# Performance work log

Measured on AMD Instinct MI355X. Metric: run time of the kernel, lower is better.

## Reference

```python
import jax, jax.numpy as jnp
import numpy as np

B, T, C, H = 4, 2048, 768, 12
D = C // H  # head_size = 64
ROPE_BASE = 10000.0


def rotary_tables(seq_len, dim, dtype=jnp.float32):
    # dim = head_size; uses dim//2 frequencies
    inv_freq = 1.0 / (ROPE_BASE ** (jnp.arange(0, dim, 2, dtype=jnp.float32) / dim))
    t = jnp.arange(seq_len, dtype=jnp.float32)
    freqs = jnp.outer(t, inv_freq)  # [T, D/2]
    return jnp.cos(freqs).astype(dtype), jnp.sin(freqs).astype(dtype)


def apply_rotary(x, cos, sin):
    # x: [B, H, T, D]; cos/sin: [T, D/2] broadcast over B,H
    d = x.shape[-1] // 2
    x1, x2 = x[..., :d], x[..., d:]
    y1 = x1 * cos + x2 * sin
    y2 = -x1 * sin + x2 * cos
    return jnp.concatenate([y1, y2], axis=-1)


def setup_inputs() -> dict:
    key = jax.random.key(0)
    ks = jax.random.split(key, 5)
    x = jax.random.normal(ks[0], (B, T, C), dtype=jnp.float32)
    W_attn = jax.random.normal(ks[1], (C, 3 * C), dtype=jnp.float32) * (1.0 / np.sqrt(C))
    b_attn = jax.random.normal(ks[2], (3 * C,), dtype=jnp.float32) * 0.02
    W_proj = jax.random.normal(ks[3], (C, C), dtype=jnp.float32) * (1.0 / np.sqrt(C))
    b_proj = jax.random.normal(ks[4], (C,), dtype=jnp.float32) * 0.02
    return {"x": x, "W_attn": W_attn, "b_attn": b_attn, "W_proj": W_proj, "b_proj": b_proj}


def reference(x, W_attn, b_attn, W_proj, b_proj):
    Bx, Tx, Cx = x.shape
    qkv = x @ W_attn + b_attn  # [B, T, 3C]
    q, k, v = jnp.split(qkv, 3, axis=-1)
    # [B, T, C] -> [B, H, T, D]
    to_heads = lambda a: a.reshape(Bx, Tx, H, D).transpose(0, 2, 1, 3)
    q, k, v = to_heads(q), to_heads(k), to_heads(v)
    cos, sin = rotary_tables(Tx, D, x.dtype)
    q = apply_rotary(q, cos, sin)
    k = apply_rotary(k, cos, sin)
    scale = 1.0 / np.sqrt(D)
    scores = jnp.einsum('bhqd,bhkd->bhqk', q, k) * scale  # [B, H, T, T]
    causal = jnp.tril(jnp.ones((Tx, Tx), dtype=bool))
    scores = jnp.where(causal, scores, jnp.finfo(scores.dtype).min)
    attn = jax.nn.softmax(scores, axis=-1)
    y = jnp.einsum('bhqk,bhkd->bhqd', attn, v)  # [B, H, T, D]
    y = y.transpose(0, 2, 1, 3).reshape(Bx, Tx, Cx)
    return y @ W_proj + b_proj
```

## Files before the change

kernel.cpp:

```cpp
#include <hip/hip_runtime.h>
#include <hip/hip_bf16.h>

#define BB 4
#define TT 2048
#define CC 768
#define HH 12
#define DD 64
#define MM (BB * TT)
#define BH (BB * HH)

typedef __bf16 bf16_t;
typedef __bf16 bf16x8 __attribute__((ext_vector_type(8)));
typedef __bf16 bf16x4 __attribute__((ext_vector_type(4)));
typedef float f32x4 __attribute__((ext_vector_type(4)));
typedef float f32x16 __attribute__((ext_vector_type(16)));

__device__ __forceinline__ float fast_exp2(float x) {
#if __has_builtin(__builtin_amdgcn_exp2f)
    return __builtin_amdgcn_exp2f(x);
#else
    return exp2f(x);
#endif
}

__device__ __forceinline__ uint32_t pk2(float lo, float hi) {
    bf16_t l = (bf16_t)lo, h = (bf16_t)hi;
    uint16_t lu = __builtin_bit_cast(uint16_t, l);
    uint16_t hu = __builtin_bit_cast(uint16_t, h);
    return ((uint32_t)hu << 16) | lu;
}

__device__ __forceinline__ void gload_lds16(const void* g, void* l) {
    __builtin_amdgcn_global_load_lds(
        (const __attribute__((address_space(1))) uint32_t*)g,
        (__attribute__((address_space(3))) uint32_t*)l, 16, 0, 0);
}

__global__ void cvt_f32_bf16(const float* __restrict__ in, bf16_t* __restrict__ out, int n4) {
    int tid = blockIdx.x * blockDim.x + threadIdx.x;
    if (tid >= n4) return;
    float4 v = ((const float4*)in)[tid];
    bf16x4 o;
    o[0] = (bf16_t)v.x; o[1] = (bf16_t)v.y; o[2] = (bf16_t)v.z; o[3] = (bf16_t)v.w;
    ((bf16x4*)out)[tid] = o;
}

__global__ void transpose_cvt(const float* __restrict__ W, bf16_t* __restrict__ WT, int K, int N) {
    __shared__ bf16_t tile[32][33];
    int k0 = blockIdx.x * 32, n0 = blockIdx.y * 32;
    int tx = threadIdx.x, ty = threadIdx.y;
#pragma unroll
    for (int r = 0; r < 4; ++r) {
        int kl = ty * 4 + r;
        tile[kl][tx] = (bf16_t)W[(size_t)(k0 + kl) * N + n0 + tx];
    }
    __syncthreads();
#pragma unroll
    for (int r = 0; r < 4; ++r) {
        int nl = ty * 4 + r;
        WT[(size_t)(n0 + nl) * K + k0 + tx] = tile[tx][nl];
    }
}

#define GEMM_CORE(A_, BT_, acc_)                                                       \
    __shared__ bf16_t As[2][128 * 32];                                                 \
    __shared__ bf16_t Bs[2][128 * 32];                                                 \
    int tid = threadIdx.x;                                                             \
    int wv = tid >> 6, lane = tid & 63, c = lane & 15, quad = lane >> 4;               \
    int wm = (wv >> 1) * 64, wn = (wv & 1) * 64;                                       \
    int m0 = blockIdx.x * 128, n0 = blockIdx.y * 128;                                  \
    int srow = wv * 32 + (lane >> 2);                                                  \
    int slot = lane & 3;                                                               \
    auto stage = [&](int buf, int k0) {                                                \
        _Pragma("unroll")                                                              \
        for (int ins = 0; ins < 2; ++ins) {                                            \
            int r = srow + ins * 16;                                                   \
            int g = (slot - ((r >> 1) & 3)) & 3;                                       \
            const bf16_t* ga = A_ + (size_t)(m0 + r) * K + k0 + g * 8;                 \
            const bf16_t* gb = BT_ + (size_t)(n0 + r) * K + k0 + g * 8;                \
            gload_lds16(ga, &As[buf][(wv * 32 + ins * 16) * 32]);                      \
            gload_lds16(gb, &Bs[buf][(wv * 32 + ins * 16) * 32]);                      \
        }                                                                              \
    };                                                                                 \
    int s_rd = (quad + ((c >> 1) & 3)) & 3;                                            \
    const int nk = K / 32;                                                             \
    stage(0, 0);                                                                       \
    for (int kt = 0; kt < nk; ++kt) {                                                  \
        __syncthreads();                                                               \
        if (kt + 1 < nk) stage((kt + 1) & 1, (kt + 1) * 32);                           \
        int buf = kt & 1;                                                              \
        bf16x8 af[4], bfr[4];                                                          \
        _Pragma("unroll")                                                              \
        for (int i = 0; i < 4; ++i) af[i] = *(const bf16x8*)&As[buf][(wm + i * 16 + c) * 32 + s_rd * 8];  \
        _Pragma("unroll")                                                              \
        for (int j = 0; j < 4; ++j) bfr[j] = *(const bf16x8*)&Bs[buf][(wn + j * 16 + c) * 32 + s_rd * 8]; \
        _Pragma("unroll")                                                              \
        for (int i = 0; i < 4; ++i)                                                    \
            _Pragma("unroll")                                                          \
            for (int j = 0; j < 4; ++j)                                                \
                acc_[i][j] = __builtin_amdgcn_mfma_f32_16x16x32_bf16(af[i], bfr[j], acc_[i][j], 0, 0, 0); \
    }

__global__ __launch_bounds__(256, 3) void gemm_qkv(
        const bf16_t* __restrict__ A, const bf16_t* __restrict__ BT,
        const float* __restrict__ bias,
        bf16_t* __restrict__ Qh, bf16_t* __restrict__ Kh, bf16_t* __restrict__ Vt) {
    const int K = 768;
    __shared__ __align__(16) bf16_t smem[17408];
    bf16_t* Asp = smem;
    bf16_t* Bsp = smem + 8192;
    int tid = threadIdx.x;
    int wv = tid >> 6, lane = tid & 63, c = lane & 15, quad = lane >> 4;
    int wm = (wv >> 1) * 64, wn = (wv & 1) * 64;
    int m0 = blockIdx.x * 128, n0 = blockIdx.y * 128;
    int srow = wv * 32 + (lane >> 2);
    int slot = lane & 3;
    auto stage = [&](int buf, int k0) {
#pragma unroll
        for (int ins = 0; ins < 2; ++ins) {
            int r = srow + ins * 16;
            int g = (slot - ((r >> 1) & 3)) & 3;
            gload_lds16(A + (size_t)(m0 + r) * K + k0 + g * 8, &Asp[buf * 4096 + (wv * 32 + ins * 16) * 32]);
            gload_lds16(BT + (size_t)(n0 + r) * K + k0 + g * 8, &Bsp[buf * 4096 + (wv * 32 + ins * 16) * 32]);
        }
    };
    int s_rd = (quad + ((c >> 1) & 3)) & 3;
    f32x4 acc[4][4] = {};
    const int nk = K / 32;
    stage(0, 0);
    for (int kt = 0; kt < nk; ++kt) {
        __syncthreads();
        if (kt + 1 < nk) stage((kt + 1) & 1, (kt + 1) * 32);
        int buf = kt & 1;
        bf16x8 af[4], bfr[4];
#pragma unroll
        for (int i = 0; i < 4; ++i) af[i] = *(const bf16x8*)&Asp[buf * 4096 + (wm + i * 16 + c) * 32 + s_rd * 8];
#pragma unroll
        for (int j = 0; j < 4; ++j) bfr[j] = *(const bf16x8*)&Bsp[buf * 4096 + (wn + j * 16 + c) * 32 + s_rd * 8];
#pragma unroll
        for (int i = 0; i < 4; ++i)
#pragma unroll
            for (int j = 0; j < 4; ++j)
                acc[i][j] = __builtin_amdgcn_mfma_f32_16x16x32_bf16(af[i], bfr[j], acc[i][j], 0, 0, 0);
    }
    __syncthreads();

    int type = n0 / 768;
    int hloc = ((n0 % 768) + wn) >> 6;
    int bidx = m0 >> 11;
    int colb = n0 + wn;
    int tb = (m0 + wm) & (TT - 1);
    bf16_t* epi = smem + wv * 4352;
    int rrow = lane >> 3, cchunk = lane & 7;

    if (type < 2) {
        const float rscale = (type == 0) ? 0.125f * 1.44269504088896f : 1.0f;
#pragma unroll
        for (int j = 0; j < 2; ++j) {
            int dlo = j * 16 + c;
            float infr = fast_exp2(-(float)dlo * 0.4152410118609828f);
            float blo = bias[colb + j * 16 + c];
            float bhi = bias[colb + (j + 2) * 16 + c];
#pragma unroll
            for (int i = 0; i < 4; ++i)
#pragma unroll
                for (int r = 0; r < 4; ++r) {
                    int lr = i * 16 + quad * 4 + r;
                    float a = acc[i][j][r] + blo;
                    float b2 = acc[i][j + 2][r] + bhi;
                    float fr = (float)(tb + lr) * infr;
                    float cs, sn;
                    __sincosf(fr, &sn, &cs);
                    epi[lr * 68 + dlo]      = (bf16_t)((a * cs + b2 * sn) * rscale);
                    epi[lr * 68 + dlo + 32] = (bf16_t)((-a * sn + b2 * cs) * rscale);
                }
        }
        bf16_t* dst = (type == 0 ? Qh : Kh) + (size_t)(bidx * HH + hloc) * TT * DD + (size_t)tb * DD;
#pragma unroll
        for (int it = 0; it < 8; ++it) {
            int row = it * 8 + rrow;
            bf16x8 v = *(const bf16x8*)&epi[row * 68 + cchunk * 8];
            *(bf16x8*)&dst[row * 64 + cchunk * 8] = v;
        }
    } else {
        int kt64 = tb >> 6;
#pragma unroll
        for (int j = 0; j < 4; ++j) {
            int dim = j * 16 + c;
            float bv = bias[colb + j * 16 + c];
            int rot = (dim & 7) * 8;
#pragma unroll
            for (int i = 0; i < 4; ++i)
#pragma unroll
                for (int r = 0; r < 4; ++r) {
                    int tin = i * 16 + quad * 4 + r;
                    epi[dim * 68 + ((tin + rot) & 63)] = (bf16_t)(acc[i][j][r] + bv);
                }
        }
        bf16_t* dstV = Vt + (size_t)(bidx * HH + hloc) * (TT / 64) * 4096 + (size_t)kt64 * 4096;
#pragma unroll
        for (int it = 0; it < 8; ++it) {
            int dim = it * 8 + rrow;
            int src = ((cchunk + (dim & 7)) & 7) * 8;
            bf16x8 v = *(const bf16x8*)&epi[dim * 68 + src];
            *(bf16x8*)&dstV[dim * 64 + cchunk * 8] = v;
        }
    }
}

__global__ __launch_bounds__(256, 3) void gemm_proj(
        const bf16_t* __restrict__ A, const bf16_t* __restrict__ BT,
        const float* __restrict__ bias, float* __restrict__ Cout) {
    const int K = 768;
    f32x4 acc[4][4] = {};
    GEMM_CORE(A, BT, acc)
#pragma unroll
    for (int j = 0; j < 4; ++j) {
        int col = n0 + wn + j * 16 + c;
        float bv = bias[col];
#pragma unroll
        for (int i = 0; i < 4; ++i) {
            int row = m0 + wm + i * 16 + quad * 4;
#pragma unroll
            for (int r = 0; r < 4; ++r)
                Cout[(size_t)(row + r) * CC + col] = acc[i][j][r] + bv;
        }
    }
}

__constant__ signed char RK_QT[20] = {11,10,9,8,15,15,7,14,14,13,13,6,12,12,5,4,3,2,1,0};
__constant__ signed char RK_PC[20] = { 2, 2,2,2, 0, 1,2, 0, 1, 0, 1,2, 0, 1,2,2,2,2,2,2};

__global__ __launch_bounds__(256, 3) void flash_attn(
        const bf16_t* __restrict__ Q, const bf16_t* __restrict__ Kc,
        const bf16_t* __restrict__ Vt, bf16_t* __restrict__ Y,
        float* __restrict__ Opart, float* __restrict__ Lpart) {
    __shared__ __align__(16) bf16_t smem[22016];
    bf16_t* KsB = smem;
    bf16_t* VsB = smem + 13824;

    int blk = blockIdx.x;
    int r = blk / 48, bh = blk - r * 48;
    int qt = RK_QT[r], pc = RK_PC[r];
    int kt0 = (pc == 1) ? (qt + 1) : 0;
    int ktend = (pc == 0) ? (qt + 1) : (2 * qt + 2);
    int nct = ktend - kt0;

    int wv = threadIdx.x >> 6, lane = threadIdx.x & 63;
    int b = bh / HH, h = bh - b * HH;
    int q31 = lane & 31, hi = lane >> 5;
    int qbw = qt * 128 + wv * 32;
    const bf16_t* Qg = Q + ((size_t)bh * TT + qbw) * DD;
    const bf16_t* Kg = Kc + (size_t)bh * TT * DD;
    const bf16_t* Vg = Vt + (size_t)bh * (TT / 64) * 4096;

    bf16x8 qf[4];
#pragma unroll
    for (int dk = 0; dk < 4; ++dk)
        qf[dk] = *(const bf16x8*)(Qg + (size_t)q31 * DD + dk * 16 + hi * 8);

    int srow = wv * 16 + (lane >> 3);
    int slot = lane & 7;
    auto stage = [&](int buf, int kt64) {
#pragma unroll
        for (int ins = 0; ins < 2; ++ins) {
            int rr = srow + ins * 8;
            int g = (slot - (rr & 7)) & 7;
            gload_lds16(Kg + (size_t)(kt64 * 64 + rr) * 64 + g * 8, &KsB[buf * 4096 + (wv * 16 + ins * 8) * 64]);
            gload_lds16(Vg + (size_t)kt64 * 4096 + rr * 64 + g * 8, &VsB[buf * 4096 + (wv * 16 + ins * 8) * 64]);
        }
    };

    f32x16 O[2] = {};
    float lsum = 0.0f;

    stage(0, kt0);

#define FA_TILE(FULL)                                                                   \
    {                                                                                   \
        int kt = kt0 + i;                                                               \
        int buf = i & 1;                                                                \
        __syncthreads();                                                                \
        if (i + 1 < nct) stage((i + 1) & 1, kt + 1);                                    \
        _Pragma("unroll")                                                               \
        for (int t32 = 0; t32 < 2; ++t32) {                                             \
            int ks = kt * 64 + t32 * 32;                                                \
            if (!(FULL) && ks > qbw) continue;                                          \
            bool masked = !(FULL) && (ks == qbw);                                       \
            f32x16 st = {};                                                             \
            __builtin_amdgcn_s_setprio(1);                                              \
            _Pragma("unroll")                                                           \
            for (int dk = 0; dk < 4; ++dk) {                                            \
                int row = t32 * 32 + q31;                                               \
                int sl = ((dk * 2 + hi) + (row & 7)) & 7;                               \
                bf16x8 kf = *(const bf16x8*)&KsB[buf * 4096 + row * 64 + sl * 8];       \
                st = __builtin_amdgcn_mfma_f32_32x32x16_bf16(kf, qf[dk], st, 0, 0, 0);  \
            }                                                                           \
            __builtin_amdgcn_s_setprio(0);                                              \
            bf16x8 vf[2][2];                                                            \
            _Pragma("unroll")                                                           \
            for (int dt = 0; dt < 2; ++dt)                                              \
                _Pragma("unroll")                                                       \
                for (int sli = 0; sli < 2; ++sli) {                                     \
                    int row = dt * 32 + q31;                                            \
                    int ch = t32 * 4 + sli * 2 + hi;                                    \
                    int sl = (ch + (row & 7)) & 7;                                      \
                    vf[dt][sli] = *(const bf16x8*)&VsB[buf * 4096 + row * 64 + sl * 8]; \
                }                                                                       \
            float p[16];                                                                \
            _Pragma("unroll")                                                           \
            for (int rr = 0; rr < 16; ++rr) {                                           \
                float e = fast_exp2(st[rr]);                                            \
                if (masked) {                                                           \
                    int keyl = (rr & 3) + 8 * (rr >> 2) + 4 * hi;                       \
                    if (keyl > q31) e = 0.0f;                                           \
                }                                                                       \
                p[rr] = e;                                                              \
            }                                                                           \
            lsum += ((((p[0] + p[1]) + (p[2] + p[3])) + ((p[4] + p[5]) + (p[6] + p[7])))\
                  + (((p[8] + p[9]) + (p[10] + p[11])) + ((p[12] + p[13]) + (p[14] + p[15])))); \
            union { uint32_t u[4]; bf16x8 v; } pb[2];                                   \
            _Pragma("unroll")                                                           \
            for (int sli = 0; sli < 2; ++sli) {                                         \
                uint32_t a0 = pk2(p[sli * 8 + 0], p[sli * 8 + 1]);                      \
                uint32_t b0 = pk2(p[sli * 8 + 2], p[sli * 8 + 3]);                      \
                uint32_t a1 = pk2(p[sli * 8 + 4], p[sli * 8 + 5]);                      \
                uint32_t b1 = pk2(p[sli * 8 + 6], p[sli * 8 + 7]);                      \
                asm("v_permlane32_swap_b32 %0, %1" : "+v"(a0), "+v"(a1));               \
                asm("v_permlane32_swap_b32 %0, %1" : "+v"(b0), "+v"(b1));               \
                pb[sli].u[0] = a0; pb[sli].u[1] = b0; pb[sli].u[2] = a1; pb[sli].u[3] = b1; \
            }                                                                           \
            __builtin_amdgcn_s_setprio(1);                                              \
            _Pragma("unroll")                                                           \
            for (int dt = 0; dt < 2; ++dt) {                                            \
                O[dt] = __builtin_amdgcn_mfma_f32_32x32x16_bf16(vf[dt][0], pb[0].v, O[dt], 0, 0, 0); \
                O[dt] = __builtin_amdgcn_mfma_f32_32x32x16_bf16(vf[dt][1], pb[1].v, O[dt], 0, 0, 0); \
            }                                                                           \
            __builtin_amdgcn_s_setprio(0);                                              \
        }                                                                               \
    }

    int nfull = 2 * qt - kt0;
    if (nfull > nct) nfull = nct;
    if (nfull < 0) nfull = 0;
    int i = 0;
    for (; i < nfull; ++i) FA_TILE(1)
    for (; i < nct; ++i) FA_TILE(0)
#undef FA_TILE

    float l = lsum;
    l += __shfl_xor(l, 32);

    if (pc == 2) {
        float inv_l = 1.0f / l;
        int row = b * TT + qbw + q31;
#pragma unroll
        for (int dt = 0; dt < 2; ++dt)
#pragma unroll
            for (int g = 0; g < 4; ++g) {
                bf16x4 ov;
#pragma unroll
                for (int rr = 0; rr < 4; ++rr) ov[rr] = (bf16_t)(O[dt][g * 4 + rr] * inv_l);
                *(bf16x4*)(Y + (size_t)row * CC + h * DD + dt * 32 + g * 8 + hi * 4) = ov;
            }
    } else {
        int pslot = bh * 4 + (qt - 12);
        int idx = pslot * 2 + pc;
        float* Op = Opart + ((size_t)idx * 128 + wv * 32 + q31) * 64;
#pragma unroll
        for (int dt = 0; dt < 2; ++dt)
#pragma unroll
            for (int g = 0; g < 4; ++g) {
                f32x4 ov;
#pragma unroll
                for (int rr = 0; rr < 4; ++rr) ov[rr] = O[dt][g * 4 + rr];
                *(f32x4*)(Op + dt * 32 + g * 8 + hi * 4) = ov;
            }
        if (hi == 0) Lpart[idx * 128 + wv * 32 + q31] = l;
    }
}

__global__ __launch_bounds__(256, 4) void combine_partials(
        const float* __restrict__ Opart, const float* __restrict__ Lpart,
        bf16_t* __restrict__ Y) {
    int pslot = blockIdx.x;
    int bh = pslot >> 2, qt = 12 + (pslot & 3);
    int b = bh / HH, h = bh - b * HH;
    int t = threadIdx.x;
    int q = t >> 1, dh = (t & 1) * 32;
    const float* p0 = Opart + ((size_t)(pslot * 2 + 0) * 128 + q) * 64 + dh;
    const float* p1 = Opart + ((size_t)(pslot * 2 + 1) * 128 + q) * 64 + dh;
    float inv = 1.0f / (Lpart[(pslot * 2 + 0) * 128 + q] + Lpart[(pslot * 2 + 1) * 128 + q]);
    bf16_t* y = Y + ((size_t)(b * TT + qt * 128 + q)) * CC + h * DD + dh;
#pragma unroll
    for (int g = 0; g < 4; ++g) {
        f32x4 a = *(const f32x4*)(p0 + g * 8);
        f32x4 a2 = *(const f32x4*)(p0 + g * 8 + 4);
        f32x4 c = *(const f32x4*)(p1 + g * 8);
        f32x4 c2 = *(const f32x4*)(p1 + g * 8 + 4);
        bf16x8 o;
#pragma unroll
        for (int rr = 0; rr < 4; ++rr) o[rr] = (bf16_t)((a[rr] + c[rr]) * inv);
#pragma unroll
        for (int rr = 0; rr < 4; ++rr) o[4 + rr] = (bf16_t)((a2[rr] + c2[rr]) * inv);
        *(bf16x8*)(y + g * 8) = o;
    }
}

extern "C" void kernel_launch(void* const* d_in, const int* in_sizes, int n_in,
                              void* d_out, int out_size, void* d_ws, size_t ws_size,
                              hipStream_t stream) {
    const float* x      = (const float*)d_in[0];
    const float* W_attn = (const float*)d_in[1];
    const float* b_attn = (const float*)d_in[2];
    const float* W_proj = (const float*)d_in[3];
    const float* b_proj = (const float*)d_in[4];
    float* out = (float*)d_out;

    unsigned char* ws = (unsigned char*)d_ws;
    size_t off = 0;
    auto alloc = [&](size_t bytes) { void* p = ws + off; off += (bytes + 255) & ~(size_t)255; return p; };
    bf16_t* xb  = (bf16_t*)alloc((size_t)MM * CC * 2);
    bf16_t* WaT = (bf16_t*)alloc((size_t)3 * CC * CC * 2);
    bf16_t* WpT = (bf16_t*)alloc((size_t)CC * CC * 2);
    bf16_t* Qh  = (bf16_t*)alloc((size_t)BH * TT * DD * 2);
    bf16_t* Kh  = (bf16_t*)alloc((size_t)BH * TT * DD * 2);
    bf16_t* Vt  = (bf16_t*)alloc((size_t)BH * TT * DD * 2);
    bf16_t* Yb  = (bf16_t*)alloc((size_t)MM * CC * 2);
    float*  Opart = (float*)alloc((size_t)192 * 2 * 128 * 64 * 4);
    float*  Lpart = (float*)alloc((size_t)192 * 2 * 128 * 4);

    cvt_f32_bf16<<<(MM * CC / 4 + 255) / 256, 256, 0, stream>>>(x, xb, MM * CC / 4);
    transpose_cvt<<<dim3(CC / 32, 3 * CC / 32), dim3(32, 8), 0, stream>>>(W_attn, WaT, CC, 3 * CC);
    transpose_cvt<<<dim3(CC / 32, CC / 32), dim3(32, 8), 0, stream>>>(W_proj, WpT, CC, CC);
    gemm_qkv<<<dim3(MM / 128, 3 * CC / 128), 256, 0, stream>>>(xb, WaT, b_attn, Qh, Kh, Vt);
    flash_attn<<<dim3(960), 256, 0, stream>>>(Qh, Kh, Vt, Yb, Opart, Lpart);
    combine_partials<<<dim3(192), 256, 0, stream>>>(Opart, Lpart, Yb);
    gemm_proj<<<dim3(MM / 128, CC / 128), 256, 0, stream>>>(Yb, WpT, b_proj, out);
}
```

Baseline: 187.7 us.

## Merge prep kernels, precompute RoPE table, fuse split-KV combine via atomic flags

Folds the x conversion and both weight transposes into one prep kernel that also builds a cos/sin table and zeroes completion flags. The QKV GEMM epilogue reads the table instead of computing sincos per element. The separate combine kernel is removed: the second flash-attention block to finish a split tile, detected with an atomic counter, merges the partials. GEMM launch bounds are raised to 4 waves per SIMD. Together this cuts launch count and epilogue transcendental work, at the cost of extra table loads, fences, and possible register pressure from the higher occupancy target.

```diff
diff --git a/kernel.cpp b/kernel.cpp
--- a/kernel.cpp
+++ b/kernel.cpp
@@ -36,29 +36,52 @@
         (__attribute__((address_space(3))) uint32_t*)l, 16, 0, 0);
 }
 
-__global__ void cvt_f32_bf16(const float* __restrict__ in, bf16_t* __restrict__ out, int n4) {
-    int tid = blockIdx.x * blockDim.x + threadIdx.x;
-    if (tid >= n4) return;
-    float4 v = ((const float4*)in)[tid];
-    bf16x4 o;
-    o[0] = (bf16_t)v.x; o[1] = (bf16_t)v.y; o[2] = (bf16_t)v.z; o[3] = (bf16_t)v.w;
-    ((bf16x4*)out)[tid] = o;
-}
-
-__global__ void transpose_cvt(const float* __restrict__ W, bf16_t* __restrict__ WT, int K, int N) {
-    __shared__ bf16_t tile[32][33];
-    int k0 = blockIdx.x * 32, n0 = blockIdx.y * 32;
-    int tx = threadIdx.x, ty = threadIdx.y;
-#pragma unroll
-    for (int r = 0; r < 4; ++r) {
-        int kl = ty * 4 + r;
-        tile[kl][tx] = (bf16_t)W[(size_t)(k0 + kl) * N + n0 + tx];
-    }
-    __syncthreads();
-#pragma unroll
-    for (int r = 0; r < 4; ++r) {
-        int nl = ty * 4 + r;
-        WT[(size_t)(n0 + nl) * K + k0 + tx] = tile[tx][nl];
+__global__ void prep(const float* __restrict__ x,
+                     const float* __restrict__ W_attn, const float* __restrict__ W_proj,
+                     bf16_t* __restrict__ xb, bf16_t* __restrict__ WaT, bf16_t* __restrict__ WpT,
+                     float* __restrict__ trig, int* __restrict__ flags) {
+    int blk = blockIdx.x;
+    if (blk < 6144) {
+        int tid = blk * 256 + threadIdx.x;
+        float4 v = ((const float4*)x)[tid];
+        bf16x4 o;
+        o[0] = (bf16_t)v.x; o[1] = (bf16_t)v.y; o[2] = (bf16_t)v.z; o[3] = (bf16_t)v.w;
+        ((bf16x4*)xb)[tid] = o;
+    } else if (blk < 6144 + 1728 + 576) {
+        bool isA = blk < 6144 + 1728;
+        int blk2 = blk - (isA ? 6144 : 6144 + 1728);
+        const float* W = isA ? W_attn : W_proj;
+        bf16_t* WT = isA ? WaT : WpT;
+        int N = isA ? 2304 : 768;
+        int k0 = (blk2 % 24) * 32, n0 = (blk2 / 24) * 32;
+        __shared__ bf16_t tile[32][33];
+        int tx = threadIdx.x & 31, ty = threadIdx.x >> 5;
+#pragma unroll
+        for (int r = 0; r < 4; ++r) {
+            int kl = ty * 4 + r;
+            tile[kl][tx] = (bf16_t)W[(size_t)(k0 + kl) * N + n0 + tx];
+        }
+        __syncthreads();
+#pragma unroll
+        for (int r = 0; r < 4; ++r) {
+            int nl = ty * 4 + r;
+            WT[(size_t)(n0 + nl) * 768 + k0 + tx] = tile[tx][nl];
+        }
+    } else {
+        int e = (blk - (6144 + 1728 + 576)) * 1024 + threadIdx.x * 4;
+        int d = e >> 11, t0 = e & 2047;
+        float infr = exp2f(-(float)d * 0.4152410118609828f);
+#pragma unroll
+        for (int r = 0; r < 4; ++r) {
+            float fr = (float)(t0 + r) * infr;
+            float sn, cs;
+            sincosf(fr, &sn, &cs);
+            trig[d * 2048 + t0 + r] = cs;
+            trig[65536 + d * 2048 + t0 + r] = sn;
+        }
+        if (e < 192 * 4) {
+            if (threadIdx.x < 192) flags[threadIdx.x] = 0;
+        }
     }
 }
 
@@ -101,9 +124,9 @@
                 acc_[i][j] = __builtin_amdgcn_mfma_f32_16x16x32_bf16(af[i], bfr[j], acc_[i][j], 0, 0, 0); \
     }
 
-__global__ __launch_bounds__(256, 3) void gemm_qkv(
+__global__ __launch_bounds__(256, 4) void gemm_qkv(
         const bf16_t* __restrict__ A, const bf16_t* __restrict__ BT,
-        const float* __restrict__ bias,
+        const float* __restrict__ bias, const float* __restrict__ trig,
         bf16_t* __restrict__ Qh, bf16_t* __restrict__ Kh, bf16_t* __restrict__ Vt) {
     const int K = 768;
     __shared__ __align__(16) bf16_t smem[17408];
@@ -158,22 +181,23 @@
 #pragma unroll
         for (int j = 0; j < 2; ++j) {
             int dlo = j * 16 + c;
-            float infr = fast_exp2(-(float)dlo * 0.4152410118609828f);
+            const float* ctab = trig + dlo * 2048 + tb;
+            const float* stab = trig + 65536 + dlo * 2048 + tb;
             float blo = bias[colb + j * 16 + c];
             float bhi = bias[colb + (j + 2) * 16 + c];
 #pragma unroll
-            for (int i = 0; i < 4; ++i)
+            for (int i = 0; i < 4; ++i) {
+                f32x4 cs4 = *(const f32x4*)(ctab + i * 16 + quad * 4);
+                f32x4 sn4 = *(const f32x4*)(stab + i * 16 + quad * 4);
 #pragma unroll
                 for (int r = 0; r < 4; ++r) {
                     int lr = i * 16 + quad * 4 + r;
                     float a = acc[i][j][r] + blo;
                     float b2 = acc[i][j + 2][r] + bhi;
-                    float fr = (float)(tb + lr) * infr;
-                    float cs, sn;
-                    __sincosf(fr, &sn, &cs);
-                    epi[lr * 68 + dlo]      = (bf16_t)((a * cs + b2 * sn) * rscale);
-                    epi[lr * 68 + dlo + 32] = (bf16_t)((-a * sn + b2 * cs) * rscale);
+                    epi[lr * 68 + dlo]      = (bf16_t)((a * cs4[r] + b2 * sn4[r]) * rscale);
+                    epi[lr * 68 + dlo + 32] = (bf16_t)((-a * sn4[r] + b2 * cs4[r]) * rscale);
                 }
+            }
         }
         bf16_t* dst = (type == 0 ? Qh : Kh) + (size_t)(bidx * HH + hloc) * TT * DD + (size_t)tb * DD;
 #pragma unroll
@@ -208,7 +232,7 @@
     }
 }
 
-__global__ __launch_bounds__(256, 3) void gemm_proj(
+__global__ __launch_bounds__(256, 4) void gemm_proj(
         const bf16_t* __restrict__ A, const bf16_t* __restrict__ BT,
         const float* __restrict__ bias, float* __restrict__ Cout) {
     const int K = 768;
@@ -234,7 +258,7 @@
 __global__ __launch_bounds__(256, 3) void flash_attn(
         const bf16_t* __restrict__ Q, const bf16_t* __restrict__ Kc,
         const bf16_t* __restrict__ Vt, bf16_t* __restrict__ Y,
-        float* __restrict__ Opart, float* __restrict__ Lpart) {
+        float* __restrict__ Opart, float* __restrict__ Lpart, int* __restrict__ flags) {
     __shared__ __align__(16) bf16_t smem[22016];
     bf16_t* KsB = smem;
     bf16_t* VsB = smem + 13824;
@@ -377,33 +401,35 @@
                 *(f32x4*)(Op + dt * 32 + g * 8 + hi * 4) = ov;
             }
         if (hi == 0) Lpart[idx * 128 + wv * 32 + q31] = l;
-    }
-}
-
-__global__ __launch_bounds__(256, 4) void combine_partials(
-        const float* __restrict__ Opart, const float* __restrict__ Lpart,
-        bf16_t* __restrict__ Y) {
-    int pslot = blockIdx.x;
-    int bh = pslot >> 2, qt = 12 + (pslot & 3);
-    int b = bh / HH, h = bh - b * HH;
-    int t = threadIdx.x;
-    int q = t >> 1, dh = (t & 1) * 32;
-    const float* p0 = Opart + ((size_t)(pslot * 2 + 0) * 128 + q) * 64 + dh;
-    const float* p1 = Opart + ((size_t)(pslot * 2 + 1) * 128 + q) * 64 + dh;
-    float inv = 1.0f / (Lpart[(pslot * 2 + 0) * 128 + q] + Lpart[(pslot * 2 + 1) * 128 + q]);
-    bf16_t* y = Y + ((size_t)(b * TT + qt * 128 + q)) * CC + h * DD + dh;
-#pragma unroll
-    for (int g = 0; g < 4; ++g) {
-        f32x4 a = *(const f32x4*)(p0 + g * 8);
-        f32x4 a2 = *(const f32x4*)(p0 + g * 8 + 4);
-        f32x4 c = *(const f32x4*)(p1 + g * 8);
-        f32x4 c2 = *(const f32x4*)(p1 + g * 8 + 4);
-        bf16x8 o;
-#pragma unroll
-        for (int rr = 0; rr < 4; ++rr) o[rr] = (bf16_t)((a[rr] + c[rr]) * inv);
-#pragma unroll
-        for (int rr = 0; rr < 4; ++rr) o[4 + rr] = (bf16_t)((a2[rr] + c2[rr]) * inv);
-        *(bf16x8*)(y + g * 8) = o;
+
+        __threadfence();
+        __syncthreads();
+        __shared__ int win_s;
+        if (threadIdx.x == 0)
+            win_s = (atomicAdd(&flags[pslot], 1) == 1);
+        __syncthreads();
+        if (win_s) {
+            __threadfence();
+            int t = threadIdx.x;
+            int q = t >> 1, dh = (t & 1) * 32;
+            const float* p0 = Opart + ((size_t)(pslot * 2 + 0) * 128 + q) * 64 + dh;
+            const float* p1 = Opart + ((size_t)(pslot * 2 + 1) * 128 + q) * 64 + dh;
+            float inv = 1.0f / (Lpart[(pslot * 2 + 0) * 128 + q] + Lpart[(pslot * 2 + 1) * 128 + q]);
+            bf16_t* y = Y + ((size_t)(b * TT + qt * 128 + q)) * CC + h * DD + dh;
+#pragma unroll
+            for (int g = 0; g < 4; ++g) {
+                f32x4 a  = *(const f32x4*)(p0 + g * 8);
+                f32x4 a2 = *(const f32x4*)(p0 + g * 8 + 4);
+                f32x4 c1 = *(const f32x4*)(p1 + g * 8);
+                f32x4 c2 = *(const f32x4*)(p1 + g * 8 + 4);
+                bf16x8 o;
+#pragma unroll
+                for (int rr = 0; rr < 4; ++rr) o[rr] = (bf16_t)((a[rr] + c1[rr]) * inv);
+#pragma unroll
+                for (int rr = 0; rr < 4; ++rr) o[4 + rr] = (bf16_t)((a2[rr] + c2[rr]) * inv);
+                *(bf16x8*)(y + g * 8) = o;
+            }
+        }
     }
 }
 
@@ -429,12 +455,11 @@
     bf16_t* Yb  = (bf16_t*)alloc((size_t)MM * CC * 2);
     float*  Opart = (float*)alloc((size_t)192 * 2 * 128 * 64 * 4);
     float*  Lpart = (float*)alloc((size_t)192 * 2 * 128 * 4);
-
-    cvt_f32_bf16<<<(MM * CC / 4 + 255) / 256, 256, 0, stream>>>(x, xb, MM * CC / 4);
-    transpose_cvt<<<dim3(CC / 32, 3 * CC / 32), dim3(32, 8), 0, stream>>>(W_attn, WaT, CC, 3 * CC);
-    transpose_cvt<<<dim3(CC / 32, CC / 32), dim3(32, 8), 0, stream>>>(W_proj, WpT, CC, CC);
-    gemm_qkv<<<dim3(MM / 128, 3 * CC / 128), 256, 0, stream>>>(xb, WaT, b_attn, Qh, Kh, Vt);
-    flash_attn<<<dim3(960), 256, 0, stream>>>(Qh, Kh, Vt, Yb, Opart, Lpart);
-    combine_partials<<<dim3(192), 256, 0, stream>>>(Opart, Lpart, Yb);
+    float*  trig  = (float*)alloc((size_t)2 * 32 * 2048 * 4);
+    int*    flags = (int*)alloc((size_t)192 * 4);
+
+    prep<<<dim3(6144 + 1728 + 576 + 64), 256, 0, stream>>>(x, W_attn, W_proj, xb, WaT, WpT, trig, flags);
+    gemm_qkv<<<dim3(MM / 128, 3 * CC / 128), 256, 0, stream>>>(xb, WaT, b_attn, trig, Qh, Kh, Vt);
+    flash_attn<<<dim3(960), 256, 0, stream>>>(Qh, Kh, Vt, Yb, Opart, Lpart, flags);
     gemm_proj<<<dim3(MM / 128, CC / 128), 256, 0, stream>>>(Yb, WpT, b_proj, out);
 }
```

Measured after the change: 273.9 us. 1.46x slower.
